# Kernel optimization log

Measured on AMD Instinct MI355X. Metric: run time of the kernel, lower is better.

The kernel has to match this reference:

```python
import jax, jax.numpy as jnp
import numpy as np

N_HEADS = 8
EPS = 1e-5  # torch nn.LayerNorm default


def layer_norm(x, g, b):
    mu = jnp.mean(x, axis=-1, keepdims=True)
    var = jnp.var(x, axis=-1, keepdims=True)
    return (x - mu) * jax.lax.rsqrt(var + EPS) * g + b


def mha(q_in, k_in, v_in, adj, Wq, bq, Wk, bk, Wv, bv, Wo, bo, g, be):
    # Standard GL-GIN / Co-guiding MultiHeadAttention: proj -> adjacency-masked
    # scaled dot-product softmax -> out proj -> residual + LayerNorm.
    # Dropout omitted (eval mode).
    B, Lq, D = q_in.shape
    Lk = k_in.shape[1]
    d_k = Wq.shape[-1] // N_HEADS
    q = (q_in @ Wq + bq).reshape(B, Lq, N_HEADS, d_k)
    k = (k_in @ Wk + bk).reshape(B, Lk, N_HEADS, d_k)
    v = (v_in @ Wv + bv).reshape(B, Lk, N_HEADS, d_k)
    scale = jnp.asarray(1.0 / np.sqrt(d_k), q_in.dtype)
    scores = jnp.einsum('bqhd,bkhd->bhqk', q, k) * scale  # [B,H,Lq,Lk]
    neg = jnp.asarray(-1e9, scores.dtype)
    scores = jnp.where(adj[:, None, :, :] == 0, neg, scores)
    attn = jax.nn.softmax(scores, axis=-1)
    out = jnp.einsum('bhqk,bkhd->bqhd', attn, v).reshape(B, Lq, N_HEADS * d_k)
    out = out @ Wo + bo
    return layer_norm(out + q_in, g, be)


def co_guiding_forward(h_a, h_b, adj_a, adj_b, adj_ab, adj_ba,
                       Wq, bq, Wk, bk, Wv, bv, Wo, bo, ln_g, ln_b):
    # Param arrays are stacked [n_layer, 4, ...], branch order: a2a, b2b, a2b, b2a.
    input_a, input_b = h_a, h_b
    n_layer = Wq.shape[0]
    for i in range(n_layer):
        def P(j):
            return (Wq[i, j], bq[i, j], Wk[i, j], bk[i, j], Wv[i, j], bv[i, j],
                    Wo[i, j], bo[i, j], ln_g[i, j], ln_b[i, j])
        a2a = mha(h_a, h_a, h_a, adj_a, *P(0))
        b2b = mha(h_b, h_b, h_b, adj_b, *P(1))
        a2b = mha(h_b, h_a, h_a, adj_ab, *P(2))
        b2a = mha(h_a, h_b, h_b, adj_ba, *P(3))
        h_a = jax.nn.relu(a2a + b2a)
        h_b = jax.nn.relu(b2b + a2b)
    return input_a + h_a, input_b + h_b


def setup_inputs():
    key = jax.random.key(0)
    ks = jax.random.split(key, 16)
    B, N, D, L = 4, 1024, 256, 2
    f = lambda k, s: jax.random.normal(k, s, dtype=jnp.float32) * 0.05
    return {
        'h_a': jax.random.normal(ks[0], (B, N, D), dtype=jnp.float32),
        'h_b': jax.random.normal(ks[1], (B, N, D), dtype=jnp.float32),
        'adj_a': jax.random.randint(ks[2], (B, N, N), 0, 2, dtype=jnp.int32),
        'adj_b': jax.random.randint(ks[3], (B, N, N), 0, 2, dtype=jnp.int32),
        'adj_ab': jax.random.randint(ks[4], (B, N, N), 0, 2, dtype=jnp.int32),
        'adj_ba': jax.random.randint(ks[5], (B, N, N), 0, 2, dtype=jnp.int32),
        'Wq': f(ks[6], (L, 4, D, D)), 'bq': f(ks[7], (L, 4, D)),
        'Wk': f(ks[8], (L, 4, D, D)), 'bk': f(ks[9], (L, 4, D)),
        'Wv': f(ks[10], (L, 4, D, D)), 'bv': f(ks[11], (L, 4, D)),
        'Wo': f(ks[12], (L, 4, D, D)), 'bo': f(ks[13], (L, 4, D)),
        'ln_g': jnp.ones((L, 4, D), dtype=jnp.float32),
        'ln_b': jnp.zeros((L, 4, D), dtype=jnp.float32),
    }


def reference(h_a, h_b, adj_a, adj_b, adj_ab, adj_ba,
              Wq, bq, Wk, bk, Wv, bv, Wo, bo, ln_g, ln_b):
    return co_guiding_forward(h_a, h_b, adj_a, adj_b, adj_ab, adj_ba,
                              Wq, bq, Wk, bk, Wv, bv, Wo, bo, ln_g, ln_b)
```

## Files before the change

### kernel.cpp

```cpp
#include <hip/hip_runtime.h>
#include <hip/hip_bf16.h>
#include <stdint.h>


using bf16x8 = __attribute__((ext_vector_type(8))) short;
using f32x4  = __attribute__((ext_vector_type(4))) float;
using f32x16 = __attribute__((ext_vector_type(16))) float;

#define DEVI __device__ __forceinline__

DEVI uint16_t f2bf(float x) {
  uint32_t u = __float_as_uint(x);
  u += 0x7FFFu + ((u >> 16) & 1u);
  return (uint16_t)(u >> 16);
}
DEVI uint32_t packbf2(float lo, float hi) {
  union { __hip_bfloat162 h; uint32_t u; } cv;
  cv.h = __float22bfloat162_rn(make_float2(lo, hi));
  return cv.u;
}
DEVI float bf2f(uint16_t v) { return __uint_as_float((uint32_t)v << 16); }
DEVI int phi4(int m) {
  return ((m & 4) << 1) | ((m & 8) >> 1) | (m & 3);
}

__global__ __launch_bounds__(256) void wprep_k(const float* __restrict__ Wq,
                                               const float* __restrict__ Wk,
                                               const float* __restrict__ Wv,
                                               const float* __restrict__ Wo,
                                               uint16_t* __restrict__ out) {
  const int z = blockIdx.z;
  const int type = z >> 3, mat = z & 7;
  const float* W = (type == 0 ? Wq : type == 1 ? Wk : type == 2 ? Wv : Wo)
                   + (size_t)mat * 65536;
  uint16_t* o = out + (size_t)type * 524288 + (size_t)mat * 65536;
  const int r0 = blockIdx.y * 64, c0 = blockIdx.x * 64;
  __shared__ float tl[64][68];
  const int t = threadIdx.x;
  {
    const int rr = t >> 2, cb = (t & 3) * 16;
    const float* src = W + (size_t)(r0 + rr) * 256 + c0 + cb;
    #pragma unroll
    for (int q = 0; q < 4; ++q) {
      float4 v = *(const float4*)(src + q * 4);
      tl[rr][cb + q*4 + 0] = v.x; tl[rr][cb + q*4 + 1] = v.y;
      tl[rr][cb + q*4 + 2] = v.z; tl[rr][cb + q*4 + 3] = v.w;
    }
  }
  __syncthreads();
  {
    const int nn = t >> 2, kb = (t & 3) * 16;
    __align__(16) uint16_t tmp[16];
    #pragma unroll
    for (int q = 0; q < 16; ++q) tmp[q] = f2bf(tl[kb + q][nn]);
    uint16_t* dst = o + (size_t)(c0 + nn) * 256 + r0 + kb;
    *(uint4*)&dst[0] = *(uint4*)&tmp[0];
    *(uint4*)&dst[8] = *(uint4*)&tmp[8];
  }
}

__global__ __launch_bounds__(256) void cvt_k(const float* __restrict__ a,
                                             const float* __restrict__ b,
                                             uint16_t* __restrict__ oa,
                                             uint16_t* __restrict__ ob) {
  const size_t i = ((size_t)blockIdx.x * 256 + threadIdx.x) * 8;
  const float* s = blockIdx.y ? b : a;
  uint16_t* o = blockIdx.y ? ob : oa;
  const float4 f0 = *(const float4*)(s + i), f1 = *(const float4*)(s + i + 4);
  uint4 u;
  u.x = packbf2(f0.x, f0.y); u.y = packbf2(f0.z, f0.w);
  u.z = packbf2(f1.x, f1.y); u.w = packbf2(f1.z, f1.w);
  *(uint4*)(o + i) = u;
}

struct AdjArgs { const int* adj[4]; uint32_t* bits[4]; };

__global__ __launch_bounds__(256) void adjbits_k(AdjArgs a) {
  const int* adj = a.adj[blockIdx.z];
  uint32_t* bits = a.bits[blockIdx.z];
  const size_t i = (size_t)blockIdx.x * 256 + threadIdx.x;
  const int lane = threadIdx.x & 63;
  const int v = adj[i];
  unsigned long long m = __ballot(v != 0);
  if ((lane & 31) == 0) {
    const uint32_t wi = (uint32_t)(i >> 5);
    const uint32_t kw = wi & 31;
    const uint32_t q  = (wi >> 5) & 1023;
    const uint32_t bb = wi >> 15;
    bits[((bb * 32 + kw) << 10) | q] = (uint32_t)(m >> (lane & 32));
  }
}

struct GemmArgs {
  const uint16_t* A[12];
  const uint16_t* W[12];
  const float*    bias[12];
  const uint16_t* res[12];
  void*           C[12];
  float           os[12];
  int             mode[12];
};

DEVI void stage_tile(const uint16_t* __restrict__ Ab,
                     const uint16_t* __restrict__ Wt,
                     int m0, int n0, int kk,
                     char* AsB, char* BsB, int wid, int lane) {
  #pragma unroll
  for (int i = 0; i < 2; ++i) {
    const int seg = i * 4 + wid;
    const int rl  = (seg << 4) + (lane >> 2);
    const int gs  = (lane & 3) ^ ((lane >> 3) & 3);
    const uint16_t* gA = Ab + (size_t)(m0 + rl) * 256 + kk + gs * 8;
    const uint16_t* gB = Wt + (size_t)(n0 + rl) * 256 + kk + gs * 8;
    __builtin_amdgcn_global_load_lds(
        (const __attribute__((address_space(1))) void*)gA,
        (__attribute__((address_space(3))) void*)(AsB + (seg << 10)), 16, 0, 0);
    __builtin_amdgcn_global_load_lds(
        (const __attribute__((address_space(1))) void*)gB,
        (__attribute__((address_space(3))) void*)(BsB + (seg << 10)), 16, 0, 0);
  }
}

__global__ __launch_bounds__(256) void gemm_k(GemmArgs args) {
  const int z  = blockIdx.z;
  const int m0 = blockIdx.y * 128, n0 = blockIdx.x * 128;
  const uint16_t* Ab = args.A[z];
  const uint16_t* Wt = args.W[z];
  __shared__ __align__(16) uint16_t As[2][4096];
  __shared__ __align__(16) uint16_t Bs[2][4096];
  const int t = threadIdx.x;
  const int lane = t & 63, wid = t >> 6;
  const int g = lane >> 4, c = lane & 15;
  const int gx = g ^ ((c >> 1) & 3);
  const int wm = (wid >> 1) * 64, wn = (wid & 1) * 64;
  f32x4 acc[4][4] = {};

  stage_tile(Ab, Wt, m0, n0, 0, (char*)As[0], (char*)Bs[0], wid, lane);
  __syncthreads();

  for (int ks = 0; ks < 8; ++ks) {
    const int buf = ks & 1;
    if (ks < 7)
      stage_tile(Ab, Wt, m0, n0, (ks + 1) * 32,
                 (char*)As[buf ^ 1], (char*)Bs[buf ^ 1], wid, lane);
    bf16x8 af[4], bfr[4];
    #pragma unroll
    for (int mt = 0; mt < 4; ++mt)
      af[mt]  = *(const bf16x8*)&As[buf][(wm + mt * 16 + c) * 32 + gx * 8];
    #pragma unroll
    for (int nt = 0; nt < 4; ++nt)
      bfr[nt] = *(const bf16x8*)&Bs[buf][(wn + nt * 16 + c) * 32 + gx * 8];
    #pragma unroll
    for (int mt = 0; mt < 4; ++mt)
      #pragma unroll
      for (int nt = 0; nt < 4; ++nt)
        acc[mt][nt] = __builtin_amdgcn_mfma_f32_16x16x32_bf16(af[mt], bfr[nt], acc[mt][nt], 0, 0, 0);
    if (ks < 7) __syncthreads();
  }

  const float* bias = args.bias[z];
  const float osz = args.os[z];
  const int mode = args.mode[z];
  float bv[4];
  #pragma unroll
  for (int nt = 0; nt < 4; ++nt) bv[nt] = bias[n0 + wn + nt * 16 + c];

  if (mode == 1) {
    const uint16_t* res = args.res[z];
    uint16_t* C = (uint16_t*)args.C[z];
    #pragma unroll
    for (int mt = 0; mt < 4; ++mt)
      #pragma unroll
      for (int r = 0; r < 4; ++r) {
        const int row = m0 + wm + mt * 16 + 4 * g + r;
        #pragma unroll
        for (int nt = 0; nt < 4; ++nt) {
          const int col = n0 + wn + nt * 16 + c;
          C[(size_t)row * 256 + col] =
              f2bf((acc[mt][nt][r] + bv[nt]) * osz + bf2f(res[(size_t)row * 256 + col]));
        }
      }
  } else if (mode == 2) {
    uint16_t* C = (uint16_t*)args.C[z];
    #pragma unroll
    for (int mt = 0; mt < 4; ++mt)
      #pragma unroll
      for (int r = 0; r < 4; ++r) {
        const int row = m0 + wm + mt * 16 + 4 * g + r;
        const int bb = row >> 10, n = row & 1023;
        #pragma unroll
        for (int nt = 0; nt < 4; ++nt) {
          const int col = n0 + wn + nt * 16 + c;
          const int hh = col >> 5, d = col & 31;
          C[((size_t)(bb * 8 + hh) * 1024 + n) * 32 + d] =
              f2bf((acc[mt][nt][r] + bv[nt]) * osz);
        }
      }
  } else {
    uint16_t* C = (uint16_t*)args.C[z];
    #pragma unroll
    for (int mt = 0; mt < 4; ++mt)
      #pragma unroll
      for (int r = 0; r < 4; ++r) {
        const int row = m0 + wm + mt * 16 + 4 * g + r;
        const int bb = row >> 10, n = row & 1023;
        const int nn = (n & ~15) | phi4(n & 15);
        #pragma unroll
        for (int nt = 0; nt < 4; ++nt) {
          const int col = n0 + wn + nt * 16 + c;
          const int hh = col >> 5, d = col & 31;
          C[((size_t)(bb * 8 + hh) * 32 + d) * 1024 + nn] =
              f2bf((acc[mt][nt][r] + bv[nt]) * osz);
        }
      }
  }
}

struct AttnArgs {
  const uint16_t* Q[4];
  const uint16_t* K[4];
  const uint16_t* Vt[4];
  const uint32_t* adjb[4];
  uint16_t*       O[4];
};

DEVI void soft_pv(f32x16& st, uint32_t w, float& l,
                  const bf16x8& vf0, const bf16x8& vf1, f32x16& oacc) {
  float s0 = 0.f, s1 = 0.f, s2 = 0.f, s3 = 0.f;
  #pragma unroll
  for (int r = 0; r < 16; ++r) {
    const int pos = (r & 3) + 8 * (r >> 2);
    const uint32_t msk = (uint32_t)__builtin_amdgcn_sbfe((int)w, pos, 1);
    const float pv = __uint_as_float(
        __float_as_uint(__builtin_amdgcn_exp2f(st[r])) & msk);
    st[r] = pv;
    if ((r & 3) == 0) s0 += pv; else if ((r & 3) == 1) s1 += pv;
    else if ((r & 3) == 2) s2 += pv; else s3 += pv;
  }
  l += (s0 + s1) + (s2 + s3);

  union PU { uint32_t u[4]; bf16x8 v; };
  PU p0, p1;
  p0.u[0] = packbf2(st[0],  st[1]);  p0.u[1] = packbf2(st[2],  st[3]);
  p0.u[2] = packbf2(st[4],  st[5]);  p0.u[3] = packbf2(st[6],  st[7]);
  p1.u[0] = packbf2(st[8],  st[9]);  p1.u[1] = packbf2(st[10], st[11]);
  p1.u[2] = packbf2(st[12], st[13]); p1.u[3] = packbf2(st[14], st[15]);

  oacc = __builtin_amdgcn_mfma_f32_32x32x16_bf16(vf0, p0.v, oacc, 0, 0, 0);
  oacc = __builtin_amdgcn_mfma_f32_32x32x16_bf16(vf1, p1.v, oacc, 0, 0, 0);
}

__global__ __launch_bounds__(256) void attn_k(AttnArgs args) {
  const int bid = blockIdx.x;
  const int qt  = bid >> 7;
  const int grp = bid & 127;
  const int bh = grp & 31, j = grp >> 5;
  const int b = bh >> 3, h = bh & 7;
  const int t = threadIdx.x, wid = t >> 6, lane = t & 63;
  const int qg = wid & 1, ks = wid >> 1;
  const int c = lane & 31, hi = lane >> 5;
  const int hsh = hi * 4;
  const int qrow = qt * 128 + qg * 64 + c;

  const uint16_t* Qbh = args.Q[j] + (size_t)(b * 8 + h) * 32768;
  const uint16_t* Kbh = args.K[j] + (size_t)(b * 8 + h) * 32768;
  const uint16_t* Vbh = args.Vt[j] + ((size_t)(b * 8 + h) * 32 + c) * 1024 + hi * 8;

  const bf16x8 qa0 = *(const bf16x8*)&Qbh[qrow * 32 + hi * 8];
  const bf16x8 qa1 = *(const bf16x8*)&Qbh[qrow * 32 + 16 + hi * 8];
  const bf16x8 qb0 = *(const bf16x8*)&Qbh[(qrow + 32) * 32 + hi * 8];
  const bf16x8 qb1 = *(const bf16x8*)&Qbh[(qrow + 32) * 32 + 16 + hi * 8];

  f32x16 oA = {}, oB = {};
  float lA = 0.f, lB = 0.f;

  const int kbeg = ks * 512;
  const uint16_t* kp = Kbh + (size_t)(kbeg + c) * 32 + hi * 8;
  const uint16_t* vp = Vbh + kbeg;
  const uint32_t* ap = args.adjb[j] + (size_t)b * 32768
                       + ((size_t)(kbeg >> 5) << 10) + qrow;

  for (int it = 0; it < 16; ++it) {
    const uint32_t wA = ap[0]  >> hsh;
    const uint32_t wB = ap[32] >> hsh;
    const bf16x8 kf0 = *(const bf16x8*)kp;
    const bf16x8 kf1 = *(const bf16x8*)(kp + 16);
    const bf16x8 vf0 = *(const bf16x8*)vp;
    const bf16x8 vf1 = *(const bf16x8*)(vp + 16);
    ap += 1024; kp += 1024; vp += 32;

    f32x16 sA = {}, sB = {};
    sA = __builtin_amdgcn_mfma_f32_32x32x16_bf16(kf0, qa0, sA, 0, 0, 0);
    sA = __builtin_amdgcn_mfma_f32_32x32x16_bf16(kf1, qa1, sA, 0, 0, 0);
    sB = __builtin_amdgcn_mfma_f32_32x32x16_bf16(kf0, qb0, sB, 0, 0, 0);
    sB = __builtin_amdgcn_mfma_f32_32x32x16_bf16(kf1, qb1, sB, 0, 0, 0);

    soft_pv(sA, wA, lA, vf0, vf1, oA);
    soft_pv(sB, wB, lB, vf0, vf1, oB);
  }

  __shared__ float red[2][2][64][17];
  if (ks == 1) {
    #pragma unroll
    for (int r = 0; r < 16; ++r) {
      red[qg][0][lane][r] = oA[r];
      red[qg][1][lane][r] = oB[r];
    }
    red[qg][0][lane][16] = lA;
    red[qg][1][lane][16] = lB;
  }
  __syncthreads();
  if (ks == 1) return;

  {
    #pragma unroll
    for (int r = 0; r < 16; ++r) {
      oA[r] += red[qg][0][lane][r];
      oB[r] += red[qg][1][lane][r];
    }
    lA += red[qg][0][lane][16];
    lB += red[qg][1][lane][16];
  }

  lA += __shfl_xor(lA, 32, 64);
  lB += __shfl_xor(lB, 32, 64);
  const float invA = 1.0f / lA;
  const float invB = 1.0f / lB;
  uint16_t* O = args.O[j];
  const size_t obA = (size_t)(b * 1024 + qrow) * 256 + h * 32 + 4 * hi;
  const size_t obB = obA + (size_t)32 * 256;
  #pragma unroll
  for (int rq = 0; rq < 4; ++rq) {
    uint2 vA, vB;
    vA.x = packbf2(oA[4*rq+0] * invA, oA[4*rq+1] * invA);
    vA.y = packbf2(oA[4*rq+2] * invA, oA[4*rq+3] * invA);
    vB.x = packbf2(oB[4*rq+0] * invB, oB[4*rq+1] * invB);
    vB.y = packbf2(oB[4*rq+2] * invB, oB[4*rq+3] * invB);
    *(uint2*)&O[obA + 8 * rq] = vA;
    *(uint2*)&O[obB + 8 * rq] = vB;
  }
}

struct LnArgs {
  const uint16_t* x0; const uint16_t* x1;
  const float* g0; const float* be0;
  const float* g1; const float* be1;
  const float* addin;
  float* out;
  uint16_t* outbf;
};
struct LnBoth { LnArgs p[2]; };

__global__ __launch_bounds__(256) void ln_k(LnBoth args) {
  const LnArgs a = args.p[blockIdx.z];
  const int wid = threadIdx.x >> 6, lane = threadIdx.x & 63;
  const int row = blockIdx.x * 4 + wid;
  const size_t off = (size_t)row * 256 + lane * 4;

  const uint2 u0 = *(const uint2*)(a.x0 + off);
  const uint2 u1 = *(const uint2*)(a.x1 + off);
  float4 x0, x1;
  x0.x = bf2f((uint16_t)u0.x); x0.y = bf2f((uint16_t)(u0.x >> 16));
  x0.z = bf2f((uint16_t)u0.y); x0.w = bf2f((uint16_t)(u0.y >> 16));
  x1.x = bf2f((uint16_t)u1.x); x1.y = bf2f((uint16_t)(u1.x >> 16));
  x1.z = bf2f((uint16_t)u1.y); x1.w = bf2f((uint16_t)(u1.y >> 16));

  float s0 = x0.x + x0.y + x0.z + x0.w;
  float s1 = x1.x + x1.y + x1.z + x1.w;
  #pragma unroll
  for (int s = 1; s < 64; s <<= 1) { s0 += __shfl_xor(s0, s, 64); s1 += __shfl_xor(s1, s, 64); }
  const float mu0 = s0 * (1.f / 256.f), mu1 = s1 * (1.f / 256.f);
  const float d0x = x0.x - mu0, d0y = x0.y - mu0, d0z = x0.z - mu0, d0w = x0.w - mu0;
  const float d1x = x1.x - mu1, d1y = x1.y - mu1, d1z = x1.z - mu1, d1w = x1.w - mu1;
  float v0 = d0x * d0x + d0y * d0y + d0z * d0z + d0w * d0w;
  float v1 = d1x * d1x + d1y * d1y + d1z * d1z + d1w * d1w;
  #pragma unroll
  for (int s = 1; s < 64; s <<= 1) { v0 += __shfl_xor(v0, s, 64); v1 += __shfl_xor(v1, s, 64); }
  const float r0 = rsqrtf(v0 * (1.f / 256.f) + 1e-5f);
  const float r1 = rsqrtf(v1 * (1.f / 256.f) + 1e-5f);

  const size_t po = (size_t)lane * 4;
  const float4 g0 = *(const float4*)(a.g0 + po), b0 = *(const float4*)(a.be0 + po);
  const float4 g1 = *(const float4*)(a.g1 + po), b1 = *(const float4*)(a.be1 + po);

  float4 y;
  y.x = fmaxf(d0x * r0 * g0.x + b0.x + d1x * r1 * g1.x + b1.x, 0.f);
  y.y = fmaxf(d0y * r0 * g0.y + b0.y + d1y * r1 * g1.y + b1.y, 0.f);
  y.z = fmaxf(d0z * r0 * g0.z + b0.z + d1z * r1 * g1.z + b1.z, 0.f);
  y.w = fmaxf(d0w * r0 * g0.w + b0.w + d1w * r1 * g1.w + b1.w, 0.f);
  if (a.addin) {
    const float4 ad = *(const float4*)(a.addin + off);
    y.x += ad.x; y.y += ad.y; y.z += ad.z; y.w += ad.w;
  }
  if (a.out) *(float4*)(a.out + off) = y;
  if (a.outbf) {
    uint2 vb;
    vb.x = packbf2(y.x, y.y); vb.y = packbf2(y.z, y.w);
    *(uint2*)(a.outbf + off) = vb;
  }
}

extern "C" void kernel_launch(void* const* d_in, const int* in_sizes, int n_in,
                              void* d_out, int out_size, void* d_ws, size_t ws_size,
                              hipStream_t stream) {
  (void)in_sizes; (void)n_in; (void)out_size; (void)ws_size;
  const float* h_a = (const float*)d_in[0];
  const float* h_b = (const float*)d_in[1];
  const float* bq  = (const float*)d_in[7];
  const float* bk  = (const float*)d_in[9];
  const float* bv  = (const float*)d_in[11];
  const float* bo  = (const float*)d_in[13];
  const float* lng = (const float*)d_in[14];
  const float* lnb = (const float*)d_in[15];

  const float QSC = 1.4426950408889634f * 0.17677669529663687f;

  char* ws = (char*)d_ws;
  uint16_t* WT   = (uint16_t*)ws;
  uint32_t* ADJB = (uint32_t*)(ws + (4u  << 20));
  uint16_t* hAbf = (uint16_t*)(ws + (6u  << 20));
  uint16_t* hBbf = (uint16_t*)(ws + (8u  << 20));
  uint16_t* Qb[4]; uint16_t* Kb[4]; uint16_t* Vtb[4]; uint16_t* ATb[4]; uint16_t* MOb[4];
  for (int j = 0; j < 4; ++j) {
    Qb[j]  = (uint16_t*)(ws + (10u << 20) + (size_t)j * (2u << 20));
    Kb[j]  = (uint16_t*)(ws + (18u << 20) + (size_t)j * (2u << 20));
    Vtb[j] = (uint16_t*)(ws + (26u << 20) + (size_t)j * (2u << 20));
    ATb[j] = (uint16_t*)(ws + (34u << 20) + (size_t)j * (2u << 20));
    MOb[j] = (uint16_t*)(ws + (42u << 20) + (size_t)j * (2u << 20));
  }

  wprep_k<<<dim3(4, 4, 32), 256, 0, stream>>>(
      (const float*)d_in[6], (const float*)d_in[8],
      (const float*)d_in[10], (const float*)d_in[12], WT);
  cvt_k<<<dim3(512, 2), 256, 0, stream>>>(h_a, h_b, hAbf, hBbf);
  {
    AdjArgs aa;
    for (int j = 0; j < 4; ++j) {
      aa.adj[j]  = (const int*)d_in[2 + j];
      aa.bits[j] = ADJB + (size_t)j * 131072;
    }
    adjbits_k<<<dim3(16384, 1, 4), 256, 0, stream>>>(aa);
  }

  for (int i = 0; i < 2; ++i) {
    const uint16_t* qbf[4]  = { hAbf, hBbf, hBbf, hAbf };
    const uint16_t* kvbf[4] = { hAbf, hBbf, hAbf, hBbf };

    {
      GemmArgs ga = {};
      for (int j = 0; j < 4; ++j) {
        const int mm = i * 4 + j;
        ga.A[j]     = qbf[j];  ga.W[j]     = WT + 0 * 524288 + (size_t)mm * 65536;
        ga.bias[j]  = bq + mm * 256; ga.C[j] = Qb[j];  ga.os[j] = QSC;  ga.mode[j] = 2;
        ga.A[4+j]   = kvbf[j]; ga.W[4+j]   = WT + 1 * 524288 + (size_t)mm * 65536;
        ga.bias[4+j]= bk + mm * 256; ga.C[4+j] = Kb[j]; ga.os[4+j] = 1.0f; ga.mode[4+j] = 2;
        ga.A[8+j]   = kvbf[j]; ga.W[8+j]   = WT + 2 * 524288 + (size_t)mm * 65536;
        ga.bias[8+j]= bv + mm * 256; ga.C[8+j] = Vtb[j]; ga.os[8+j] = 1.0f; ga.mode[8+j] = 3;
      }
      gemm_k<<<dim3(2, 32, 12), 256, 0, stream>>>(ga);
    }
    {
      AttnArgs at;
      for (int j = 0; j < 4; ++j) {
        at.Q[j] = Qb[j]; at.K[j] = Kb[j]; at.Vt[j] = Vtb[j];
        at.adjb[j] = ADJB + (size_t)j * 131072; at.O[j] = ATb[j];
      }
      attn_k<<<dim3(1024, 1, 1), 256, 0, stream>>>(at);
    }
    {
      GemmArgs go = {};
      for (int j = 0; j < 4; ++j) {
        const int mm = i * 4 + j;
        go.A[j] = ATb[j]; go.W[j] = WT + 3 * 524288 + (size_t)mm * 65536;
        go.bias[j] = bo + mm * 256; go.res[j] = qbf[j]; go.C[j] = MOb[j];
        go.os[j] = 1.0f; go.mode[j] = 1;
      }
      gemm_k<<<dim3(2, 32, 4), 256, 0, stream>>>(go);
    }
    {
      LnBoth lb;
      float* outA = (i == 1) ? (float*)d_out : nullptr;
      float* outB = (i == 1) ? ((float*)d_out + 1048576) : nullptr;
      const float* addA = (i == 1) ? h_a : nullptr;
      const float* addB = (i == 1) ? h_b : nullptr;
      uint16_t* mbA = (i == 0) ? hAbf : nullptr;
      uint16_t* mbB = (i == 0) ? hBbf : nullptr;
      lb.p[0] = { MOb[0], MOb[3],
                  lng + (i * 4 + 0) * 256, lnb + (i * 4 + 0) * 256,
                  lng + (i * 4 + 3) * 256, lnb + (i * 4 + 3) * 256,
                  addA, outA, mbA };
      lb.p[1] = { MOb[1], MOb[2],
                  lng + (i * 4 + 1) * 256, lnb + (i * 4 + 1) * 256,
                  lng + (i * 4 + 2) * 256, lnb + (i * 4 + 2) * 256,
                  addB, outB, mbB };
      ln_k<<<dim3(1024, 1, 2), 256, 0, stream>>>(lb);
    }
  }
}
```

Measured before the change: 200.6 us.

## Stage GEMM head-layout epilogues through LDS and double query rows per attention block

The QKV GEMM epilogues for the Q/K head-major layout and the transposed V layout now write tiles into shared memory first, then issue 16-byte vectorized global stores instead of scattered 2-byte stores. The attention kernel processes 256 query rows per block (four 32-row groups per wave instead of two), halving the grid so each loaded K/V fragment is reused across more queries. The larger per-wave state raises register pressure and halves block count, which may reduce occupancy on the attention kernel.

After: 211.3 us. 1.05x slower.

```diff
diff --git a/kernel.cpp b/kernel.cpp
--- a/kernel.cpp
+++ b/kernel.cpp
@@ -182,37 +182,48 @@
       }
   } else if (mode == 2) {
     uint16_t* C = (uint16_t*)args.C[z];
-    #pragma unroll
-    for (int mt = 0; mt < 4; ++mt)
+    __syncthreads();
+    uint16_t* ep = ((uint16_t*)As) + wid * (16 * 72);
+    #pragma unroll
+    for (int mt = 0; mt < 4; ++mt) {
+      #pragma unroll
+      for (int r = 0; r < 4; ++r)
+        #pragma unroll
+        for (int nt = 0; nt < 4; ++nt)
+          ep[(4 * g + r) * 72 + nt * 16 + c] = f2bf((acc[mt][nt][r] + bv[nt]) * osz);
+      #pragma unroll
+      for (int sr = 0; sr < 2; ++sr) {
+        const int row  = sr * 8 + (lane >> 3);
+        const int col8 = (lane & 7) * 8;
+        const uint4 v4 = *(const uint4*)&ep[row * 72 + col8];
+        const int n  = m0 + wm + mt * 16 + row;
+        const int bb = n >> 10, nn = n & 1023;
+        const int colg = n0 + wn + col8;
+        const int hh = colg >> 5, d = colg & 31;
+        *(uint4*)&C[((size_t)(bb * 8 + hh) * 1024 + nn) * 32 + d] = v4;
+      }
+    }
+  } else {
+    uint16_t* C = (uint16_t*)args.C[z];
+    __syncthreads();
+    uint16_t* ep = ((uint16_t*)As) + wid * (64 * 24);
+    const int colg = n0 + wn + lane;
+    const int hh = colg >> 5, d = colg & 31;
+    #pragma unroll
+    for (int mt = 0; mt < 4; ++mt) {
       #pragma unroll
       for (int r = 0; r < 4; ++r) {
-        const int row = m0 + wm + mt * 16 + 4 * g + r;
-        const int bb = row >> 10, n = row & 1023;
+        const int pn = phi4(4 * g + r);
         #pragma unroll
-        for (int nt = 0; nt < 4; ++nt) {
-          const int col = n0 + wn + nt * 16 + c;
-          const int hh = col >> 5, d = col & 31;
-          C[((size_t)(bb * 8 + hh) * 1024 + n) * 32 + d] =
-              f2bf((acc[mt][nt][r] + bv[nt]) * osz);
-        }
+        for (int nt = 0; nt < 4; ++nt)
+          ep[(nt * 16 + c) * 24 + pn] = f2bf((acc[mt][nt][r] + bv[nt]) * osz);
       }
-  } else {
-    uint16_t* C = (uint16_t*)args.C[z];
-    #pragma unroll
-    for (int mt = 0; mt < 4; ++mt)
-      #pragma unroll
-      for (int r = 0; r < 4; ++r) {
-        const int row = m0 + wm + mt * 16 + 4 * g + r;
-        const int bb = row >> 10, n = row & 1023;
-        const int nn = (n & ~15) | phi4(n & 15);
-        #pragma unroll
-        for (int nt = 0; nt < 4; ++nt) {
-          const int col = n0 + wn + nt * 16 + c;
-          const int hh = col >> 5, d = col & 31;
-          C[((size_t)(bb * 8 + hh) * 32 + d) * 1024 + nn] =
-              f2bf((acc[mt][nt][r] + bv[nt]) * osz);
-        }
-      }
+      const int nbase = m0 + wm + mt * 16;
+      const int bb = nbase >> 10, nb = nbase & 1023;
+      uint16_t* dst = C + ((size_t)(bb * 8 + hh) * 32 + d) * 1024 + nb;
+      *(uint4*)dst       = *(const uint4*)&ep[lane * 24];
+      *(uint4*)(dst + 8) = *(const uint4*)&ep[lane * 24 + 8];
+    }
   }
 }
 
@@ -260,7 +271,7 @@
   const int qg = wid & 1, ks = wid >> 1;
   const int c = lane & 31, hi = lane >> 5;
   const int hsh = hi * 4;
-  const int qrow = qt * 128 + qg * 64 + c;
+  const int qrow = qt * 256 + qg * 128 + c;
 
   const uint16_t* Qbh = args.Q[j] + (size_t)(b * 8 + h) * 32768;
   const uint16_t* Kbh = args.K[j] + (size_t)(b * 8 + h) * 32768;
@@ -270,9 +281,13 @@
   const bf16x8 qa1 = *(const bf16x8*)&Qbh[qrow * 32 + 16 + hi * 8];
   const bf16x8 qb0 = *(const bf16x8*)&Qbh[(qrow + 32) * 32 + hi * 8];
   const bf16x8 qb1 = *(const bf16x8*)&Qbh[(qrow + 32) * 32 + 16 + hi * 8];
-
-  f32x16 oA = {}, oB = {};
-  float lA = 0.f, lB = 0.f;
+  const bf16x8 qc0 = *(const bf16x8*)&Qbh[(qrow + 64) * 32 + hi * 8];
+  const bf16x8 qc1 = *(const bf16x8*)&Qbh[(qrow + 64) * 32 + 16 + hi * 8];
+  const bf16x8 qd0 = *(const bf16x8*)&Qbh[(qrow + 96) * 32 + hi * 8];
+  const bf16x8 qd1 = *(const bf16x8*)&Qbh[(qrow + 96) * 32 + 16 + hi * 8];
+
+  f32x16 oA = {}, oB = {}, oC = {}, oD = {};
+  float lA = 0.f, lB = 0.f, lC = 0.f, lD = 0.f;
 
   const int kbeg = ks * 512;
   const uint16_t* kp = Kbh + (size_t)(kbeg + c) * 32 + hi * 8;
@@ -283,6 +298,8 @@
   for (int it = 0; it < 16; ++it) {
     const uint32_t wA = ap[0]  >> hsh;
     const uint32_t wB = ap[32] >> hsh;
+    const uint32_t wC = ap[64] >> hsh;
+    const uint32_t wD = ap[96] >> hsh;
     const bf16x8 kf0 = *(const bf16x8*)kp;
     const bf16x8 kf1 = *(const bf16x8*)(kp + 16);
     const bf16x8 vf0 = *(const bf16x8*)vp;
@@ -294,20 +311,31 @@
     sA = __builtin_amdgcn_mfma_f32_32x32x16_bf16(kf1, qa1, sA, 0, 0, 0);
     sB = __builtin_amdgcn_mfma_f32_32x32x16_bf16(kf0, qb0, sB, 0, 0, 0);
     sB = __builtin_amdgcn_mfma_f32_32x32x16_bf16(kf1, qb1, sB, 0, 0, 0);
-
     soft_pv(sA, wA, lA, vf0, vf1, oA);
     soft_pv(sB, wB, lB, vf0, vf1, oB);
-  }
-
-  __shared__ float red[2][2][64][17];
+
+    f32x16 sC = {}, sD = {};
+    sC = __builtin_amdgcn_mfma_f32_32x32x16_bf16(kf0, qc0, sC, 0, 0, 0);
+    sC = __builtin_amdgcn_mfma_f32_32x32x16_bf16(kf1, qc1, sC, 0, 0, 0);
+    sD = __builtin_amdgcn_mfma_f32_32x32x16_bf16(kf0, qd0, sD, 0, 0, 0);
+    sD = __builtin_amdgcn_mfma_f32_32x32x16_bf16(kf1, qd1, sD, 0, 0, 0);
+    soft_pv(sC, wC, lC, vf0, vf1, oC);
+    soft_pv(sD, wD, lD, vf0, vf1, oD);
+  }
+
+  __shared__ float red[2][4][64][17];
   if (ks == 1) {
     #pragma unroll
     for (int r = 0; r < 16; ++r) {
       red[qg][0][lane][r] = oA[r];
       red[qg][1][lane][r] = oB[r];
+      red[qg][2][lane][r] = oC[r];
+      red[qg][3][lane][r] = oD[r];
     }
     red[qg][0][lane][16] = lA;
     red[qg][1][lane][16] = lB;
+    red[qg][2][lane][16] = lC;
+    red[qg][3][lane][16] = lD;
   }
   __syncthreads();
   if (ks == 1) return;
@@ -317,27 +345,37 @@
     for (int r = 0; r < 16; ++r) {
       oA[r] += red[qg][0][lane][r];
       oB[r] += red[qg][1][lane][r];
+      oC[r] += red[qg][2][lane][r];
+      oD[r] += red[qg][3][lane][r];
     }
     lA += red[qg][0][lane][16];
     lB += red[qg][1][lane][16];
+    lC += red[qg][2][lane][16];
+    lD += red[qg][3][lane][16];
   }
 
   lA += __shfl_xor(lA, 32, 64);
   lB += __shfl_xor(lB, 32, 64);
-  const float invA = 1.0f / lA;
-  const float invB = 1.0f / lB;
+  lC += __shfl_xor(lC, 32, 64);
+  lD += __shfl_xor(lD, 32, 64);
+  const float iA = 1.0f / lA, iB = 1.0f / lB, iC = 1.0f / lC, iD = 1.0f / lD;
   uint16_t* O = args.O[j];
-  const size_t obA = (size_t)(b * 1024 + qrow) * 256 + h * 32 + 4 * hi;
-  const size_t obB = obA + (size_t)32 * 256;
+  const size_t ob = (size_t)(b * 1024 + qrow) * 256 + h * 32 + 4 * hi;
   #pragma unroll
   for (int rq = 0; rq < 4; ++rq) {
-    uint2 vA, vB;
-    vA.x = packbf2(oA[4*rq+0] * invA, oA[4*rq+1] * invA);
-    vA.y = packbf2(oA[4*rq+2] * invA, oA[4*rq+3] * invA);
-    vB.x = packbf2(oB[4*rq+0] * invB, oB[4*rq+1] * invB);
-    vB.y = packbf2(oB[4*rq+2] * invB, oB[4*rq+3] * invB);
-    *(uint2*)&O[obA + 8 * rq] = vA;
-    *(uint2*)&O[obB + 8 * rq] = vB;
+    uint2 v;
+    v.x = packbf2(oA[4*rq+0] * iA, oA[4*rq+1] * iA);
+    v.y = packbf2(oA[4*rq+2] * iA, oA[4*rq+3] * iA);
+    *(uint2*)&O[ob + 8 * rq] = v;
+    v.x = packbf2(oB[4*rq+0] * iB, oB[4*rq+1] * iB);
+    v.y = packbf2(oB[4*rq+2] * iB, oB[4*rq+3] * iB);
+    *(uint2*)&O[ob + (size_t)32 * 256 + 8 * rq] = v;
+    v.x = packbf2(oC[4*rq+0] * iC, oC[4*rq+1] * iC);
+    v.y = packbf2(oC[4*rq+2] * iC, oC[4*rq+3] * iC);
+    *(uint2*)&O[ob + (size_t)64 * 256 + 8 * rq] = v;
+    v.x = packbf2(oD[4*rq+0] * iD, oD[4*rq+1] * iD);
+    v.y = packbf2(oD[4*rq+2] * iD, oD[4*rq+3] * iD);
+    *(uint2*)&O[ob + (size_t)96 * 256 + 8 * rq] = v;
   }
 }
 
@@ -465,7 +503,7 @@
         at.Q[j] = Qb[j]; at.K[j] = Kb[j]; at.Vt[j] = Vtb[j];
         at.adjb[j] = ADJB + (size_t)j * 131072; at.O[j] = ATb[j];
       }
-      attn_k<<<dim3(1024, 1, 1), 256, 0, stream>>>(at);
+      attn_k<<<dim3(512, 1, 1), 256, 0, stream>>>(at);
     }
     {
       GemmArgs go = {};
```

## Fuse output projection, residual and dual LayerNorm; coalesce QKV epilogue via LDS

Applied to the files above, without the earlier changes.

Replaces the separate output-projection GEMM and LayerNorm kernels with one kernel, opln_k. Each block computes both branch projections for 32 rows against full weight tiles, adds bias and residual, and does both LayerNorms, the ReLU sum and the final residual or bf16 write-back in registers and LDS. This removes the intermediate MOb buffers and one launch per layer. Separately, the QKV GEMM epilogue is staged through LDS so the Q/K and transposed-V outputs are written as 16-byte vector stores instead of scattered 2-byte stores. In exchange, every block re-reads both whole 256x256 weight matrices, grid occupancy is small at 256 blocks with large LDS, and variance is now computed as E[x^2]-mu^2.

Result: faster. 192.9 us (-3.8%).

```diff
diff --git a/kernel.cpp b/kernel.cpp
--- a/kernel.cpp
+++ b/kernel.cpp
@@ -95,7 +95,6 @@
   const uint16_t* A[12];
   const uint16_t* W[12];
   const float*    bias[12];
-  const uint16_t* res[12];
   void*           C[12];
   float           os[12];
   int             mode[12];
@@ -165,54 +164,50 @@
   #pragma unroll
   for (int nt = 0; nt < 4; ++nt) bv[nt] = bias[n0 + wn + nt * 16 + c];
 
-  if (mode == 1) {
-    const uint16_t* res = args.res[z];
+  if (mode == 2) {
     uint16_t* C = (uint16_t*)args.C[z];
-    #pragma unroll
-    for (int mt = 0; mt < 4; ++mt)
-      #pragma unroll
-      for (int r = 0; r < 4; ++r) {
-        const int row = m0 + wm + mt * 16 + 4 * g + r;
+    __syncthreads();
+    uint16_t* ep = ((uint16_t*)As) + wid * (16 * 72);
+    #pragma unroll
+    for (int mt = 0; mt < 4; ++mt) {
+      #pragma unroll
+      for (int r = 0; r < 4; ++r)
         #pragma unroll
-        for (int nt = 0; nt < 4; ++nt) {
-          const int col = n0 + wn + nt * 16 + c;
-          C[(size_t)row * 256 + col] =
-              f2bf((acc[mt][nt][r] + bv[nt]) * osz + bf2f(res[(size_t)row * 256 + col]));
-        }
-      }
-  } else if (mode == 2) {
-    uint16_t* C = (uint16_t*)args.C[z];
-    #pragma unroll
-    for (int mt = 0; mt < 4; ++mt)
-      #pragma unroll
-      for (int r = 0; r < 4; ++r) {
-        const int row = m0 + wm + mt * 16 + 4 * g + r;
-        const int bb = row >> 10, n = row & 1023;
-        #pragma unroll
-        for (int nt = 0; nt < 4; ++nt) {
-          const int col = n0 + wn + nt * 16 + c;
-          const int hh = col >> 5, d = col & 31;
-          C[((size_t)(bb * 8 + hh) * 1024 + n) * 32 + d] =
-              f2bf((acc[mt][nt][r] + bv[nt]) * osz);
-        }
-      }
+        for (int nt = 0; nt < 4; ++nt)
+          ep[(4 * g + r) * 72 + nt * 16 + c] = f2bf((acc[mt][nt][r] + bv[nt]) * osz);
+      #pragma unroll
+      for (int sr = 0; sr < 2; ++sr) {
+        const int row  = sr * 8 + (lane >> 3);
+        const int col8 = (lane & 7) * 8;
+        const uint4 v4 = *(const uint4*)&ep[row * 72 + col8];
+        const int n  = m0 + wm + mt * 16 + row;
+        const int bb = n >> 10, nn = n & 1023;
+        const int colg = n0 + wn + col8;
+        const int hh = colg >> 5, d = colg & 31;
+        *(uint4*)&C[((size_t)(bb * 8 + hh) * 1024 + nn) * 32 + d] = v4;
+      }
+    }
   } else {
     uint16_t* C = (uint16_t*)args.C[z];
-    #pragma unroll
-    for (int mt = 0; mt < 4; ++mt)
+    __syncthreads();
+    uint16_t* ep = ((uint16_t*)As) + wid * (64 * 24);
+    const int colg = n0 + wn + lane;
+    const int hh = colg >> 5, d = colg & 31;
+    #pragma unroll
+    for (int mt = 0; mt < 4; ++mt) {
       #pragma unroll
       for (int r = 0; r < 4; ++r) {
-        const int row = m0 + wm + mt * 16 + 4 * g + r;
-        const int bb = row >> 10, n = row & 1023;
-        const int nn = (n & ~15) | phi4(n & 15);
+        const int pn = phi4(4 * g + r);
         #pragma unroll
-        for (int nt = 0; nt < 4; ++nt) {
-          const int col = n0 + wn + nt * 16 + c;
-          const int hh = col >> 5, d = col & 31;
-          C[((size_t)(bb * 8 + hh) * 32 + d) * 1024 + nn] =
-              f2bf((acc[mt][nt][r] + bv[nt]) * osz);
-        }
-      }
+        for (int nt = 0; nt < 4; ++nt)
+          ep[(nt * 16 + c) * 24 + pn] = f2bf((acc[mt][nt][r] + bv[nt]) * osz);
+      }
+      const int nbase = m0 + wm + mt * 16;
+      const int bb = nbase >> 10, nb = nbase & 1023;
+      uint16_t* dst = C + ((size_t)(bb * 8 + hh) * 32 + d) * 1024 + nb;
+      *(uint4*)dst       = *(const uint4*)&ep[lane * 24];
+      *(uint4*)(dst + 8) = *(const uint4*)&ep[lane * 24 + 8];
+    }
   }
 }
 
@@ -341,62 +336,199 @@
   }
 }
 
-struct LnArgs {
-  const uint16_t* x0; const uint16_t* x1;
-  const float* g0; const float* be0;
-  const float* g1; const float* be1;
-  const float* addin;
-  float* out;
-  uint16_t* outbf;
+struct OplnArgs {
+  const uint16_t* A0[2]; const uint16_t* A1[2];
+  const uint16_t* W0[2]; const uint16_t* W1[2];
+  const float*    b0[2]; const float*    b1[2];
+  const uint16_t* res[2];
+  const float* g0[2]; const float* be0[2];
+  const float* g1[2]; const float* be1[2];
+  const float* addin[2];
+  float*     outf[2];
+  uint16_t*  outbf[2];
 };
-struct LnBoth { LnArgs p[2]; };
-
-__global__ __launch_bounds__(256) void ln_k(LnBoth args) {
-  const LnArgs a = args.p[blockIdx.z];
-  const int wid = threadIdx.x >> 6, lane = threadIdx.x & 63;
-  const int row = blockIdx.x * 4 + wid;
-  const size_t off = (size_t)row * 256 + lane * 4;
-
-  const uint2 u0 = *(const uint2*)(a.x0 + off);
-  const uint2 u1 = *(const uint2*)(a.x1 + off);
-  float4 x0, x1;
-  x0.x = bf2f((uint16_t)u0.x); x0.y = bf2f((uint16_t)(u0.x >> 16));
-  x0.z = bf2f((uint16_t)u0.y); x0.w = bf2f((uint16_t)(u0.y >> 16));
-  x1.x = bf2f((uint16_t)u1.x); x1.y = bf2f((uint16_t)(u1.x >> 16));
-  x1.z = bf2f((uint16_t)u1.y); x1.w = bf2f((uint16_t)(u1.y >> 16));
-
-  float s0 = x0.x + x0.y + x0.z + x0.w;
-  float s1 = x1.x + x1.y + x1.z + x1.w;
-  #pragma unroll
-  for (int s = 1; s < 64; s <<= 1) { s0 += __shfl_xor(s0, s, 64); s1 += __shfl_xor(s1, s, 64); }
-  const float mu0 = s0 * (1.f / 256.f), mu1 = s1 * (1.f / 256.f);
-  const float d0x = x0.x - mu0, d0y = x0.y - mu0, d0z = x0.z - mu0, d0w = x0.w - mu0;
-  const float d1x = x1.x - mu1, d1y = x1.y - mu1, d1z = x1.z - mu1, d1w = x1.w - mu1;
-  float v0 = d0x * d0x + d0y * d0y + d0z * d0z + d0w * d0w;
-  float v1 = d1x * d1x + d1y * d1y + d1z * d1z + d1w * d1w;
-  #pragma unroll
-  for (int s = 1; s < 64; s <<= 1) { v0 += __shfl_xor(v0, s, 64); v1 += __shfl_xor(v1, s, 64); }
-  const float r0 = rsqrtf(v0 * (1.f / 256.f) + 1e-5f);
-  const float r1 = rsqrtf(v1 * (1.f / 256.f) + 1e-5f);
-
-  const size_t po = (size_t)lane * 4;
-  const float4 g0 = *(const float4*)(a.g0 + po), b0 = *(const float4*)(a.be0 + po);
-  const float4 g1 = *(const float4*)(a.g1 + po), b1 = *(const float4*)(a.be1 + po);
-
-  float4 y;
-  y.x = fmaxf(d0x * r0 * g0.x + b0.x + d1x * r1 * g1.x + b1.x, 0.f);
-  y.y = fmaxf(d0y * r0 * g0.y + b0.y + d1y * r1 * g1.y + b1.y, 0.f);
-  y.z = fmaxf(d0z * r0 * g0.z + b0.z + d1z * r1 * g1.z + b1.z, 0.f);
-  y.w = fmaxf(d0w * r0 * g0.w + b0.w + d1w * r1 * g1.w + b1.w, 0.f);
-  if (a.addin) {
-    const float4 ad = *(const float4*)(a.addin + off);
-    y.x += ad.x; y.y += ad.y; y.z += ad.z; y.w += ad.w;
-  }
-  if (a.out) *(float4*)(a.out + off) = y;
-  if (a.outbf) {
-    uint2 vb;
-    vb.x = packbf2(y.x, y.y); vb.y = packbf2(y.z, y.w);
-    *(uint2*)(a.outbf + off) = vb;
+
+__global__ __launch_bounds__(256) void opln_k(OplnArgs args) {
+  const int side = blockIdx.y;
+  const int m0 = blockIdx.x * 32;
+  const uint16_t* A0 = args.A0[side];
+  const uint16_t* A1 = args.A1[side];
+  const uint16_t* W0 = args.W0[side];
+  const uint16_t* W1 = args.W1[side];
+
+  __shared__ __align__(16) char lds[76800];
+  uint16_t* As0 = (uint16_t*)(lds);
+  uint16_t* As1 = (uint16_t*)(lds + 4096);
+  uint16_t* Bs0 = (uint16_t*)(lds + 8192);
+  uint16_t* Bs1 = (uint16_t*)(lds + 8192 + 32768);
+  float*    red = (float*)(lds + 8192 + 65536);
+  float*    muv = (float*)(lds + 8192 + 65536 + 2048);
+  uint16_t* outt = (uint16_t*)lds;
+
+  const int t = threadIdx.x;
+  const int lane = t & 63, wid = t >> 6;
+  const int g = lane >> 4, c = lane & 15;
+  const int gx = g ^ ((c >> 1) & 3);
+  const int gs = (lane & 3) ^ ((lane >> 3) & 3);
+
+  auto stage = [&](int buf, int kk) {
+    {
+      const uint16_t* src = (wid < 2) ? A0 : A1;
+      char* dst = (char*)((wid < 2) ? As0 : As1) + (size_t)buf * 2048 + ((wid & 1) << 10);
+      const int rl = ((wid & 1) << 4) + (lane >> 2);
+      __builtin_amdgcn_global_load_lds(
+          (const __attribute__((address_space(1))) void*)(src + (size_t)(m0 + rl) * 256 + kk + gs * 8),
+          (__attribute__((address_space(3))) void*)dst, 16, 0, 0);
+    }
+    #pragma unroll
+    for (int i = 0; i < 8; ++i) {
+      const int s32 = i * 4 + wid;
+      const int mat = s32 >> 4, seg = s32 & 15;
+      const uint16_t* src = mat ? W1 : W0;
+      char* dst = (char*)(mat ? Bs1 : Bs0) + (size_t)buf * 16384 + (seg << 10);
+      const int rl = (seg << 4) + (lane >> 2);
+      __builtin_amdgcn_global_load_lds(
+          (const __attribute__((address_space(1))) void*)(src + (size_t)rl * 256 + kk + gs * 8),
+          (__attribute__((address_space(3))) void*)dst, 16, 0, 0);
+    }
+  };
+
+  f32x4 a0[2][4] = {}, a1[2][4] = {};
+  stage(0, 0);
+  __syncthreads();
+
+  for (int ks = 0; ks < 8; ++ks) {
+    const int buf = ks & 1;
+    if (ks < 7) stage(buf ^ 1, (ks + 1) * 32);
+    const uint16_t* As0b = As0 + buf * 1024;
+    const uint16_t* As1b = As1 + buf * 1024;
+    const uint16_t* Bs0b = Bs0 + buf * 8192;
+    const uint16_t* Bs1b = Bs1 + buf * 8192;
+    bf16x8 fa0[2], fa1[2], fb0[4], fb1[4];
+    #pragma unroll
+    for (int mt = 0; mt < 2; ++mt) {
+      fa0[mt] = *(const bf16x8*)&As0b[(mt * 16 + c) * 32 + gx * 8];
+      fa1[mt] = *(const bf16x8*)&As1b[(mt * 16 + c) * 32 + gx * 8];
+    }
+    #pragma unroll
+    for (int nt = 0; nt < 4; ++nt) {
+      fb0[nt] = *(const bf16x8*)&Bs0b[(wid * 64 + nt * 16 + c) * 32 + gx * 8];
+      fb1[nt] = *(const bf16x8*)&Bs1b[(wid * 64 + nt * 16 + c) * 32 + gx * 8];
+    }
+    #pragma unroll
+    for (int mt = 0; mt < 2; ++mt)
+      #pragma unroll
+      for (int nt = 0; nt < 4; ++nt) {
+        a0[mt][nt] = __builtin_amdgcn_mfma_f32_16x16x32_bf16(fa0[mt], fb0[nt], a0[mt][nt], 0, 0, 0);
+        a1[mt][nt] = __builtin_amdgcn_mfma_f32_16x16x32_bf16(fa1[mt], fb1[nt], a1[mt][nt], 0, 0, 0);
+      }
+    if (ks < 7) __syncthreads();
+  }
+
+  const float* b0p = args.b0[side];
+  const float* b1p = args.b1[side];
+  const uint16_t* resp = args.res[side];
+  float bv0[4], bv1[4];
+  #pragma unroll
+  for (int nt = 0; nt < 4; ++nt) {
+    bv0[nt] = b0p[wid * 64 + nt * 16 + c];
+    bv1[nt] = b1p[wid * 64 + nt * 16 + c];
+  }
+  #pragma unroll
+  for (int mt = 0; mt < 2; ++mt)
+    #pragma unroll
+    for (int r = 0; r < 4; ++r) {
+      const int row = mt * 16 + 4 * g + r;
+      #pragma unroll
+      for (int nt = 0; nt < 4; ++nt) {
+        const float rf = bf2f(resp[(size_t)(m0 + row) * 256 + wid * 64 + nt * 16 + c]);
+        a0[mt][nt][r] = a0[mt][nt][r] + bv0[nt] + rf;
+        a1[mt][nt][r] = a1[mt][nt][r] + bv1[nt] + rf;
+      }
+    }
+
+  #pragma unroll
+  for (int mt = 0; mt < 2; ++mt)
+    #pragma unroll
+    for (int r = 0; r < 4; ++r) {
+      float s0 = 0.f, ss0 = 0.f, s1 = 0.f, ss1 = 0.f;
+      #pragma unroll
+      for (int nt = 0; nt < 4; ++nt) {
+        const float x0 = a0[mt][nt][r], x1 = a1[mt][nt][r];
+        s0 += x0; ss0 += x0 * x0; s1 += x1; ss1 += x1 * x1;
+      }
+      #pragma unroll
+      for (int m = 1; m < 16; m <<= 1) {
+        s0 += __shfl_xor(s0, m, 64);  ss0 += __shfl_xor(ss0, m, 64);
+        s1 += __shfl_xor(s1, m, 64);  ss1 += __shfl_xor(ss1, m, 64);
+      }
+      if (c == 0) {
+        const int row = mt * 16 + 4 * g + r;
+        float* rp = red + (row * 4 + wid) * 4;
+        rp[0] = s0; rp[1] = ss0; rp[2] = s1; rp[3] = ss1;
+      }
+    }
+  __syncthreads();
+
+  if (t < 32) {
+    float S0 = 0.f, SS0 = 0.f, S1 = 0.f, SS1 = 0.f;
+    #pragma unroll
+    for (int w = 0; w < 4; ++w) {
+      const float* rp = red + (t * 4 + w) * 4;
+      S0 += rp[0]; SS0 += rp[1]; S1 += rp[2]; SS1 += rp[3];
+    }
+    const float mu0 = S0 * (1.f / 256.f);
+    const float mu1 = S1 * (1.f / 256.f);
+    const float rs0 = rsqrtf(SS0 * (1.f / 256.f) - mu0 * mu0 + 1e-5f);
+    const float rs1 = rsqrtf(SS1 * (1.f / 256.f) - mu1 * mu1 + 1e-5f);
+    float* mp = muv + t * 4;
+    mp[0] = mu0; mp[1] = rs0; mp[2] = mu1; mp[3] = rs1;
+  }
+  __syncthreads();
+
+  const float* g0p = args.g0[side];  const float* be0p = args.be0[side];
+  const float* g1p = args.g1[side];  const float* be1p = args.be1[side];
+  float ga0[4], bb0[4], ga1[4], bb1[4];
+  #pragma unroll
+  for (int nt = 0; nt < 4; ++nt) {
+    const int col = wid * 64 + nt * 16 + c;
+    ga0[nt] = g0p[col]; bb0[nt] = be0p[col];
+    ga1[nt] = g1p[col]; bb1[nt] = be1p[col];
+  }
+  #pragma unroll
+  for (int mt = 0; mt < 2; ++mt)
+    #pragma unroll
+    for (int r = 0; r < 4; ++r) {
+      const int row = mt * 16 + 4 * g + r;
+      const float4 m4 = *(const float4*)(muv + row * 4);
+      #pragma unroll
+      for (int nt = 0; nt < 4; ++nt) {
+        const float y = fmaxf((a0[mt][nt][r] - m4.x) * m4.y * ga0[nt] + bb0[nt]
+                            + (a1[mt][nt][r] - m4.z) * m4.w * ga1[nt] + bb1[nt], 0.f);
+        outt[row * 272 + wid * 64 + nt * 16 + c] = f2bf(y);
+      }
+    }
+  __syncthreads();
+
+  const int orow = t >> 3, ocb = (t & 7) * 32;
+  if (args.addin[side]) {
+    const float* ad = args.addin[side] + (size_t)(m0 + orow) * 256 + ocb;
+    float* of = args.outf[side] + (size_t)(m0 + orow) * 256 + ocb;
+    #pragma unroll
+    for (int q = 0; q < 8; ++q) {
+      const float4 av = *(const float4*)(ad + q * 4);
+      float4 y4;
+      y4.x = bf2f(outt[orow * 272 + ocb + q * 4 + 0]) + av.x;
+      y4.y = bf2f(outt[orow * 272 + ocb + q * 4 + 1]) + av.y;
+      y4.z = bf2f(outt[orow * 272 + ocb + q * 4 + 2]) + av.z;
+      y4.w = bf2f(outt[orow * 272 + ocb + q * 4 + 3]) + av.w;
+      *(float4*)(of + q * 4) = y4;
+    }
+  } else {
+    uint16_t* ob = args.outbf[side] + (size_t)(m0 + orow) * 256 + ocb;
+    #pragma unroll
+    for (int q = 0; q < 4; ++q)
+      *(uint4*)(ob + q * 8) = *(const uint4*)&outt[orow * 272 + ocb + q * 8];
   }
 }
 
@@ -420,13 +552,12 @@
   uint32_t* ADJB = (uint32_t*)(ws + (4u  << 20));
   uint16_t* hAbf = (uint16_t*)(ws + (6u  << 20));
   uint16_t* hBbf = (uint16_t*)(ws + (8u  << 20));
-  uint16_t* Qb[4]; uint16_t* Kb[4]; uint16_t* Vtb[4]; uint16_t* ATb[4]; uint16_t* MOb[4];
+  uint16_t* Qb[4]; uint16_t* Kb[4]; uint16_t* Vtb[4]; uint16_t* ATb[4];
   for (int j = 0; j < 4; ++j) {
     Qb[j]  = (uint16_t*)(ws + (10u << 20) + (size_t)j * (2u << 20));
     Kb[j]  = (uint16_t*)(ws + (18u << 20) + (size_t)j * (2u << 20));
     Vtb[j] = (uint16_t*)(ws + (26u << 20) + (size_t)j * (2u << 20));
     ATb[j] = (uint16_t*)(ws + (34u << 20) + (size_t)j * (2u << 20));
-    MOb[j] = (uint16_t*)(ws + (42u << 20) + (size_t)j * (2u << 20));
   }
 
   wprep_k<<<dim3(4, 4, 32), 256, 0, stream>>>(
@@ -468,32 +599,28 @@
       attn_k<<<dim3(1024, 1, 1), 256, 0, stream>>>(at);
     }
     {
-      GemmArgs go = {};
-      for (int j = 0; j < 4; ++j) {
-        const int mm = i * 4 + j;
-        go.A[j] = ATb[j]; go.W[j] = WT + 3 * 524288 + (size_t)mm * 65536;
-        go.bias[j] = bo + mm * 256; go.res[j] = qbf[j]; go.C[j] = MOb[j];
-        go.os[j] = 1.0f; go.mode[j] = 1;
-      }
-      gemm_k<<<dim3(2, 32, 4), 256, 0, stream>>>(go);
-    }
-    {
-      LnBoth lb;
-      float* outA = (i == 1) ? (float*)d_out : nullptr;
-      float* outB = (i == 1) ? ((float*)d_out + 1048576) : nullptr;
-      const float* addA = (i == 1) ? h_a : nullptr;
-      const float* addB = (i == 1) ? h_b : nullptr;
-      uint16_t* mbA = (i == 0) ? hAbf : nullptr;
-      uint16_t* mbB = (i == 0) ? hBbf : nullptr;
-      lb.p[0] = { MOb[0], MOb[3],
-                  lng + (i * 4 + 0) * 256, lnb + (i * 4 + 0) * 256,
-                  lng + (i * 4 + 3) * 256, lnb + (i * 4 + 3) * 256,
-                  addA, outA, mbA };
-      lb.p[1] = { MOb[1], MOb[2],
-                  lng + (i * 4 + 1) * 256, lnb + (i * 4 + 1) * 256,
-                  lng + (i * 4 + 2) * 256, lnb + (i * 4 + 2) * 256,
-                  addB, outB, mbB };
-      ln_k<<<dim3(1024, 1, 2), 256, 0, stream>>>(lb);
-    }
-  }
-}
+      OplnArgs oa;
+      const int j0[2] = {0, 1}, j1[2] = {3, 2};
+      for (int s = 0; s < 2; ++s) {
+        const int mm0 = i * 4 + j0[s], mm1 = i * 4 + j1[s];
+        oa.A0[s] = ATb[j0[s]];  oa.A1[s] = ATb[j1[s]];
+        oa.W0[s] = WT + 3 * 524288 + (size_t)mm0 * 65536;
+        oa.W1[s] = WT + 3 * 524288 + (size_t)mm1 * 65536;
+        oa.b0[s] = bo + mm0 * 256;  oa.b1[s] = bo + mm1 * 256;
+        oa.res[s] = s ? hBbf : hAbf;
+        oa.g0[s] = lng + mm0 * 256;  oa.be0[s] = lnb + mm0 * 256;
+        oa.g1[s] = lng + mm1 * 256;  oa.be1[s] = lnb + mm1 * 256;
+        if (i == 1) {
+          oa.addin[s] = s ? h_b : h_a;
+          oa.outf[s]  = (float*)d_out + (size_t)s * 1048576;
+          oa.outbf[s] = nullptr;
+        } else {
+          oa.addin[s] = nullptr;
+          oa.outf[s]  = nullptr;
+          oa.outbf[s] = s ? hBbf : hAbf;
+        }
+      }
+      opln_k<<<dim3(128, 2), 256, 0, stream>>>(oa);
+    }
+  }
+}
```
